# Kernel optimization log

Hardware: AMD Instinct MI355X
Metric: run time of the kernel (lower is better)

Reference implementation:

```python
import jax, jax.numpy as jnp
import numpy as np

B, T, DQ, DV, A, F, K = 64, 1024, 1024, 512, 512, 32, 31


def setup_inputs() -> dict:
    key = jax.random.key(0)
    ks = jax.random.split(key, 8)
    query = jax.random.normal(ks[0], (B, DQ), jnp.float32)
    values = jax.random.normal(ks[1], (B, T, DV), jnp.float32)
    # decoder-step states (as produced by init_states)
    attention_cum = jnp.zeros((B, T), jnp.float32)
    attention_old = jnp.zeros((B, T), jnp.float32)
    alpha = jnp.concatenate([jnp.ones((B, 1), jnp.float32),
                             jnp.zeros((B, T - 1), jnp.float32) + 1e-7], axis=1)
    # learned parameters (Glorot-ish scaling)
    W_query = jax.random.normal(ks[2], (DQ, A), jnp.float32) / np.sqrt(DQ)
    W_inputs = jax.random.normal(ks[3], (DV, A), jnp.float32) / np.sqrt(DV)
    v_w = jax.random.normal(ks[4], (A, 1), jnp.float32) / np.sqrt(A)
    v_b = jnp.zeros((1,), jnp.float32)
    loc_kernel = jax.random.normal(ks[5], (K, 2, F), jnp.float32) / np.sqrt(K * 2)  # WIO
    W_loc = jax.random.normal(ks[6], (F, A), jnp.float32) / np.sqrt(F)
    return {"query": query, "values": values, "attention_cum": attention_cum,
            "attention_old": attention_old, "alpha": alpha,
            "W_query": W_query, "W_inputs": W_inputs, "v_w": v_w, "v_b": v_b,
            "loc_kernel": loc_kernel, "W_loc": W_loc}


def reference(query, values, attention_cum, attention_old, alpha,
              W_query, W_inputs, v_w, v_b, loc_kernel, W_loc):
    # process_values: cached projection of encoder memory  [B,T,A]
    processed_values = jnp.einsum('btd,da->bta', values, W_inputs)
    # location features: conv over stacked (old, cum) attention  [B,T,2]->[B,T,F]
    attn_cat = jnp.stack([attention_old, attention_cum], axis=2)
    conv = jax.lax.conv_general_dilated(attn_cat, loc_kernel, window_strides=(1,),
                                        padding='SAME',
                                        dimension_numbers=('NWC', 'WIO', 'NWC'))
    processed_attn = jnp.einsum('btf,fa->bta', conv, W_loc)
    # query projection  [B,1,A]
    processed_query = (query @ W_query)[:, None, :]
    # additive score  [B,T]
    score = (jnp.tanh(processed_values + processed_query + processed_attn) @ v_w)[..., 0] + v_b
    scores_norm = jax.nn.softmax(score, axis=-1)
    # forward attention recursion
    fwd_shifted = jnp.pad(alpha[:, :-1], ((0, 0), (1, 0)))
    new_alpha = (0.5 * alpha + 0.5 * fwd_shifted + 1e-8) * scores_norm
    new_alpha = new_alpha / jnp.sum(new_alpha, axis=1, keepdims=True)
    attn_weights = new_alpha
    # updated states
    new_cum = attention_cum + scores_norm
    new_old = attn_weights
    # context vector  [B,DV]
    context = jnp.einsum('bt,btd->bd', attn_weights, values)
    return (context, attn_weights, new_cum, new_old, new_alpha)
```

## Files before the change

### kernel.cpp

```cpp
#include <hip/hip_runtime.h>
#include <hip/hip_bf16.h>
#include <cstdint>
#include <cstddef>

#define B 64
#define T 1024
#define DQ 1024
#define DV 512
#define A_DIM 512
#define F_DIM 32
#define KW 31
#define M_TOT (B*T)
#define KEXT2 576
#define NCH 9

typedef __attribute__((ext_vector_type(8))) short short8;
typedef __attribute__((ext_vector_type(4))) float f32x4;

static __device__ __forceinline__ unsigned short f2bf(float f) {
    unsigned int u = __builtin_bit_cast(unsigned int, f);
    u += 0x7fffu + ((u >> 16) & 1u);
    return (unsigned short)(u >> 16);
}
static __device__ __forceinline__ short8 pack8(float4 x0, float4 x1) {
    short8 pk;
    pk[0] = (short)f2bf(x0.x); pk[1] = (short)f2bf(x0.y);
    pk[2] = (short)f2bf(x0.z); pk[3] = (short)f2bf(x0.w);
    pk[4] = (short)f2bf(x1.x); pk[5] = (short)f2bf(x1.y);
    pk[6] = (short)f2bf(x1.z); pk[7] = (short)f2bf(x1.w);
    return pk;
}
static __device__ __forceinline__ float tanh_fast(float x) {
    float e = __expf(2.0f * x);
    return 1.0f - 2.0f * __builtin_amdgcn_rcpf(e + 1.0f);
}

#define LDSDMA16(gptr, lptr)                                                        \
    __builtin_amdgcn_global_load_lds(                                               \
        (const __attribute__((address_space(1))) void*)(const void*)(gptr),         \
        (__attribute__((address_space(3))) void*)(void*)(lptr), 16, 0, 0)

__global__ void prep_kernel(const float* __restrict__ query, const float* __restrict__ Wq,
                            const float* __restrict__ Wi, const float* __restrict__ Wl,
                            const float* __restrict__ old_, const float* __restrict__ cum_,
                            const float* __restrict__ lk,
                            float* __restrict__ pq,
                            float* __restrict__ score, unsigned short* __restrict__ Bt,
                            unsigned short* __restrict__ convb) {
    __shared__ __align__(16) char smem[16640];
    int bid = blockIdx.x, tid = threadIdx.x;
    if (bid < 512) {
        float (*red)[64] = (float(*)[64])smem;
        int pid = bid;
        int gid = pid * 256 + tid;
        if (gid < M_TOT) score[gid] = 0.f;
        int b = pid >> 3, a0 = (pid & 7) * 64;
        int al = tid & 63, ks = tid >> 6;
        const float* qr = query + (size_t)b * DQ + ks * 256;
        const float* wc = Wq + (size_t)(ks * 256) * A_DIM + a0 + al;
        float acc = 0.f;
        #pragma unroll 8
        for (int k = 0; k < 256; ++k) acc += qr[k] * wc[(size_t)k * A_DIM];
        red[ks][al] = acc;
        __syncthreads();
        if (ks == 0)
            pq[b * A_DIM + a0 + al] = red[0][al] + red[1][al] + red[2][al] + red[3][al];
    } else if (bid < 584) {
        float (*tile)[65] = (float(*)[65])smem;
        int tb = bid - 512;
        if (tb < 64) {
            int k0 = (tb >> 3) * 64, a0 = (tb & 7) * 64;
            int al = tid & 63, ko = tid >> 6;
            #pragma unroll
            for (int j = 0; j < 16; ++j) {
                int kl = j * 4 + ko;
                tile[kl][al] = Wi[(size_t)(k0 + kl) * A_DIM + a0 + al];
            }
            __syncthreads();
            int kl2 = tid & 63, ao = tid >> 6;
            #pragma unroll
            for (int j = 0; j < 16; ++j) {
                int al2 = j * 4 + ao;
                Bt[(size_t)(a0 + al2) * KEXT2 + k0 + kl2] = f2bf(tile[kl2][al2]);
            }
        } else {
            int a0 = (tb - 64) * 64;
            int al = tid & 63, ko = tid >> 6;
            #pragma unroll
            for (int j = 0; j < 8; ++j) {
                int kl = j * 4 + ko;
                tile[kl][al] = Wl[(size_t)kl * A_DIM + a0 + al];
            }
            __syncthreads();
            int kl2 = tid & 31, ao = tid >> 5;
            #pragma unroll
            for (int j = 0; j < 8; ++j) {
                int al2 = j * 8 + ao;
                Bt[(size_t)(a0 + al2) * KEXT2 + DV + kl2] = f2bf(tile[kl2][al2]);
            }
            #pragma unroll
            for (int j = 0; j < 8; ++j) {
                int idx = j * 256 + tid;
                int a_l = idx >> 5, kp = idx & 31;
                Bt[(size_t)(a0 + a_l) * KEXT2 + 544 + kp] = 0;
            }
        }
    } else {
        float* sOld = (float*)smem;
        float* sCum = sOld + 94;
        float* sLK  = sCum + 94;
        int cid = bid - 584;
        int b = cid >> 4, t0 = (cid & 15) * 64;
        int tl = tid & 63, fg = tid >> 6;
        for (int j = tid; j < 94; j += 256) {
            int tt = t0 - 15 + j;
            bool ok = (tt >= 0 && tt < T);
            sOld[j] = ok ? old_[b * T + tt] : 0.f;
            sCum[j] = ok ? cum_[b * T + tt] : 0.f;
        }
        for (int j = tid; j < KW * 2 * F_DIM; j += 256) sLK[j] = lk[j];
        __syncthreads();
        float acc[8];
        #pragma unroll
        for (int f = 0; f < 8; ++f) acc[f] = 0.f;
        for (int k = 0; k < KW; ++k) {
            float o = sOld[tl + k], c = sCum[tl + k];
            const float* lo = &sLK[(k * 2 + 0) * F_DIM + fg * 8];
            const float* lc = &sLK[(k * 2 + 1) * F_DIM + fg * 8];
            #pragma unroll
            for (int f = 0; f < 8; ++f) acc[f] += o * lo[f] + c * lc[f];
        }
        short8 pk;
        #pragma unroll
        for (int f = 0; f < 8; ++f) pk[f] = (short)f2bf(acc[f]);
        unsigned short* dst = convb + (size_t)(b * T + t0 + tl) * 64 + fg * 8;
        *(short8*)dst = pk;
        *(short8*)(dst + 32) = (short8)0;
    }
}

__launch_bounds__(256, 3)
__global__ void gemm_score(const float* __restrict__ values,
                           const unsigned short* __restrict__ Bt,
                           const unsigned short* __restrict__ convb,
                           const float* __restrict__ pq,
                           const float* __restrict__ vw,
                           float* __restrict__ score) {
    __shared__ __align__(16) short sA[128 * 64];
    __shared__ __align__(16) short sB[128 * 64];
    __shared__ float sPQ[128];
    __shared__ float sVW[128];
    int tid = threadIdx.x;
    int x = blockIdx.x & 7, l = blockIdx.x >> 3;
    int mt = x * 64 + (l >> 2), nq = l & 3;
    int m0 = mt * 128, n0 = nq * 128;
    int b = m0 >> 10;
    if (tid < 128) { sPQ[tid] = pq[b * A_DIM + n0 + tid]; sVW[tid] = vw[n0 + tid]; }
    int w = tid >> 6, lane = tid & 63, q = lane >> 4, l15 = lane & 15;
    int wm = w & 1, wn = w >> 1;
    const float* aSrc[4];
    int aSlot[4];
    #pragma unroll
    for (int jj = 0; jj < 4; ++jj) {
        int slot = tid * 4 + jj;
        int row = slot >> 3, sl = slot & 7, seg = (sl - row) & 7;
        aSrc[jj] = values + (size_t)(m0 + row) * DV + seg * 8;
        aSlot[jj] = slot;
    }
    f32x4 acc[4][4];
    #pragma unroll
    for (int mi = 0; mi < 4; ++mi)
        #pragma unroll
        for (int ni = 0; ni < 4; ++ni) acc[mi][ni] = (f32x4)0.f;

    for (int c = 0; c < NCH; ++c) {
        __syncthreads();
        #pragma unroll
        for (int j = 0; j < 4; ++j) {
            int slot = j * 256 + tid;
            int row = slot >> 3, seg = ((slot & 7) - row) & 7;
            const unsigned short* gB = Bt + (size_t)(n0 + row) * KEXT2 + c * 64 + seg * 8;
            LDSDMA16(gB, &sB[(j * 256 + w * 64) * 8]);
        }
        if (c < 8) {
            float4 x0[4], x1[4];
            #pragma unroll
            for (int jj = 0; jj < 4; ++jj) {
                const float* s0 = aSrc[jj] + c * 64;
                x0[jj] = *(const float4*)s0;
                x1[jj] = *(const float4*)(s0 + 4);
            }
            #pragma unroll
            for (int jj = 0; jj < 4; ++jj)
                *(short8*)&sA[aSlot[jj] * 8] = pack8(x0[jj], x1[jj]);
        } else {
            #pragma unroll
            for (int j = 0; j < 4; ++j) {
                int slot = j * 256 + tid;
                int row = slot >> 3, seg = ((slot & 7) - row) & 7;
                LDSDMA16(convb + (size_t)(m0 + row) * 64 + seg * 8,
                         &sA[(j * 256 + w * 64) * 8]);
            }
        }
        __syncthreads();
        #pragma unroll
        for (int h = 0; h < 2; ++h) {
            short8 af[4], bfr[4];
            int sgl = h * 4 + q;
            #pragma unroll
            for (int mi = 0; mi < 4; ++mi) {
                int r = wm * 64 + mi * 16 + l15;
                af[mi] = *(const short8*)&sA[r * 64 + (((sgl + r) & 7) << 3)];
            }
            #pragma unroll
            for (int ni = 0; ni < 4; ++ni) {
                int r = wn * 64 + ni * 16 + l15;
                bfr[ni] = *(const short8*)&sB[r * 64 + (((sgl + r) & 7) << 3)];
            }
            #pragma unroll
            for (int mi = 0; mi < 4; ++mi)
                #pragma unroll
                for (int ni = 0; ni < 4; ++ni)
                    acc[mi][ni] = __builtin_amdgcn_mfma_f32_16x16x32_bf16(af[mi], bfr[ni], acc[mi][ni], 0, 0, 0);
        }
    }
    #pragma unroll
    for (int mi = 0; mi < 4; ++mi) {
        #pragma unroll
        for (int r = 0; r < 4; ++r) {
            float s = 0.f;
            #pragma unroll
            for (int ni = 0; ni < 4; ++ni) {
                int col = wn * 64 + ni * 16 + l15;
                float xv = acc[mi][ni][r] + sPQ[col];
                s += tanh_fast(xv) * sVW[col];
            }
            #pragma unroll
            for (int off = 1; off < 16; off <<= 1) s += __shfl_xor(s, off, 64);
            if (l15 == 0)
                atomicAdd(&score[m0 + wm * 64 + mi * 16 + q * 4 + r], s);
        }
    }
}

__global__ void softmax_fwd(const float* __restrict__ score,
                            const float* __restrict__ alpha,
                            const float* __restrict__ cum,
                            float* __restrict__ out) {
    int b = blockIdx.x, t = threadIdx.x;
    __shared__ float sred[16];
    __shared__ float sbc;
    float sc = score[b * T + t];
    int wid = t >> 6, lane = t & 63;
    float m = sc;
    #pragma unroll
    for (int off = 32; off; off >>= 1) m = fmaxf(m, __shfl_xor(m, off, 64));
    if (lane == 0) sred[wid] = m;
    __syncthreads();
    if (t == 0) { float mm = sred[0]; for (int i = 1; i < 16; ++i) mm = fmaxf(mm, sred[i]); sbc = mm; }
    __syncthreads();
    float M = sbc;
    float e = __expf(sc - M);
    float s = e;
    #pragma unroll
    for (int off = 32; off; off >>= 1) s += __shfl_xor(s, off, 64);
    __syncthreads();
    if (lane == 0) sred[wid] = s;
    __syncthreads();
    if (t == 0) { float ss = 0.f; for (int i = 0; i < 16; ++i) ss += sred[i]; sbc = ss; }
    __syncthreads();
    float sn = e / sbc;
    float a_t = alpha[b * T + t];
    float a_p = (t > 0) ? alpha[b * T + t - 1] : 0.f;
    float ua = (0.5f * (a_t + a_p) + 1e-8f) * sn;
    float u = ua;
    #pragma unroll
    for (int off = 32; off; off >>= 1) u += __shfl_xor(u, off, 64);
    __syncthreads();
    if (lane == 0) sred[wid] = u;
    __syncthreads();
    if (t == 0) { float ss = 0.f; for (int i = 0; i < 16; ++i) ss += sred[i]; sbc = ss; }
    __syncthreads();
    float wgt = ua / sbc;
    float* attnw  = out + B * DV;
    float* ncum   = attnw + B * T;
    float* nold   = ncum + B * T;
    float* nalpha = nold + B * T;
    attnw[b * T + t]  = wgt;
    ncum[b * T + t]   = cum[b * T + t] + sn;
    nold[b * T + t]   = wgt;
    nalpha[b * T + t] = wgt;
    if (t < DV) out[b * DV + t] = 0.f;
}

__global__ void context_kernel(const float* __restrict__ values,
                               float* __restrict__ out) {
    __shared__ float red[4][256];
    const float* attnw = out + B * DV;
    int b = blockIdx.x >> 3, tq = (blockIdx.x >> 1) & 3, dh = blockIdx.x & 1;
    int sub = threadIdx.x >> 6, dg = threadIdx.x & 63;
    int t0 = tq * 256 + sub * 64;
    int d0 = dh * 256 + dg * 4;
    float acc[4];
    #pragma unroll
    for (int f = 0; f < 4; ++f) acc[f] = 0.f;
    for (int tt = 0; tt < 64; ++tt) {
        int t = t0 + tt;
        float wgt = attnw[b * T + t];
        float4 xv = *(const float4*)(values + (size_t)(b * T + t) * DV + d0);
        acc[0] += wgt * xv.x; acc[1] += wgt * xv.y;
        acc[2] += wgt * xv.z; acc[3] += wgt * xv.w;
    }
    #pragma unroll
    for (int f = 0; f < 4; ++f) red[sub][dg * 4 + f] = acc[f];
    __syncthreads();
    if (sub == 0) {
        #pragma unroll
        for (int f = 0; f < 4; ++f) {
            int di = dg * 4 + f;
            float s = red[0][di] + red[1][di] + red[2][di] + red[3][di];
            atomicAdd(&out[b * DV + dh * 256 + di], s);
        }
    }
}

extern "C" void kernel_launch(void* const* d_in, const int* in_sizes, int n_in,
                              void* d_out, int out_size, void* d_ws, size_t ws_size,
                              hipStream_t stream) {
    const float* query  = (const float*)d_in[0];
    const float* values = (const float*)d_in[1];
    const float* cum    = (const float*)d_in[2];
    const float* old_   = (const float*)d_in[3];
    const float* alpha  = (const float*)d_in[4];
    const float* Wq     = (const float*)d_in[5];
    const float* Wi     = (const float*)d_in[6];
    const float* vw     = (const float*)d_in[7];
    const float* lk     = (const float*)d_in[9];
    const float* Wl     = (const float*)d_in[10];
    float* out = (float*)d_out;
    char* ws = (char*)d_ws;
    float* ws_pq            = (float*)(ws);
    float* ws_score         = (float*)(ws + 131072);
    unsigned short* ws_Bt   = (unsigned short*)(ws + 393216);
    unsigned short* ws_conv = (unsigned short*)(ws + 1048576);

    prep_kernel<<<1608, 256, 0, stream>>>(query, Wq, Wi, Wl, old_, cum, lk,
                                          ws_pq, ws_score, ws_Bt, ws_conv);
    gemm_score<<<2048, 256, 0, stream>>>(values, ws_Bt, ws_conv, ws_pq, vw, ws_score);
    softmax_fwd<<<64, 1024, 0, stream>>>(ws_score, alpha, cum, out);
    context_kernel<<<512, 256, 0, stream>>>(values, out);
}
```

Baseline: 324.3 us.

## Double-buffer LDS tiles in gemm_score to overlap loads with MFMA

```diff
diff --git a/kernel.cpp b/kernel.cpp
--- a/kernel.cpp
+++ b/kernel.cpp
@@ -139,15 +139,15 @@
     }
 }
 
-__launch_bounds__(256, 3)
+__launch_bounds__(256, 2)
 __global__ void gemm_score(const float* __restrict__ values,
                            const unsigned short* __restrict__ Bt,
                            const unsigned short* __restrict__ convb,
                            const float* __restrict__ pq,
                            const float* __restrict__ vw,
                            float* __restrict__ score) {
-    __shared__ __align__(16) short sA[128 * 64];
-    __shared__ __align__(16) short sB[128 * 64];
+    __shared__ __align__(16) short sA[2][128 * 64];
+    __shared__ __align__(16) short sB[2][128 * 64];
     __shared__ float sPQ[128];
     __shared__ float sVW[128];
     int tid = threadIdx.x;
@@ -159,13 +159,15 @@
     int w = tid >> 6, lane = tid & 63, q = lane >> 4, l15 = lane & 15;
     int wm = w & 1, wn = w >> 1;
     const float* aSrc[4];
+    const unsigned short* bSrc[4];
     int aSlot[4];
     #pragma unroll
-    for (int jj = 0; jj < 4; ++jj) {
-        int slot = tid * 4 + jj;
-        int row = slot >> 3, sl = slot & 7, seg = (sl - row) & 7;
-        aSrc[jj] = values + (size_t)(m0 + row) * DV + seg * 8;
-        aSlot[jj] = slot;
+    for (int j = 0; j < 4; ++j) {
+        int slot = j * 256 + tid;
+        int row = slot >> 3, seg = ((slot & 7) - row) & 7;
+        aSrc[j] = values + (size_t)(m0 + row) * DV + seg * 8;
+        bSrc[j] = Bt + (size_t)(n0 + row) * KEXT2 + seg * 8;
+        aSlot[j] = slot;
     }
     f32x4 acc[4][4];
     #pragma unroll
@@ -173,36 +175,47 @@
         #pragma unroll
         for (int ni = 0; ni < 4; ++ni) acc[mi][ni] = (f32x4)0.f;
 
+    {
+        float4 px0[4], px1[4];
+        #pragma unroll
+        for (int j = 0; j < 4; ++j) {
+            px0[j] = *(const float4*)(aSrc[j]);
+            px1[j] = *(const float4*)(aSrc[j] + 4);
+        }
+        #pragma unroll
+        for (int j = 0; j < 4; ++j)
+            LDSDMA16(bSrc[j], &sB[0][(j * 256 + w * 64) * 8]);
+        #pragma unroll
+        for (int j = 0; j < 4; ++j)
+            *(short8*)&sA[0][aSlot[j] * 8] = pack8(px0[j], px1[j]);
+    }
+    __syncthreads();
+
+    int cur = 0;
     for (int c = 0; c < NCH; ++c) {
-        __syncthreads();
-        #pragma unroll
-        for (int j = 0; j < 4; ++j) {
-            int slot = j * 256 + tid;
-            int row = slot >> 3, seg = ((slot & 7) - row) & 7;
-            const unsigned short* gB = Bt + (size_t)(n0 + row) * KEXT2 + c * 64 + seg * 8;
-            LDSDMA16(gB, &sB[(j * 256 + w * 64) * 8]);
-        }
-        if (c < 8) {
-            float4 x0[4], x1[4];
-            #pragma unroll
-            for (int jj = 0; jj < 4; ++jj) {
-                const float* s0 = aSrc[jj] + c * 64;
-                x0[jj] = *(const float4*)s0;
-                x1[jj] = *(const float4*)(s0 + 4);
-            }
-            #pragma unroll
-            for (int jj = 0; jj < 4; ++jj)
-                *(short8*)&sA[aSlot[jj] * 8] = pack8(x0[jj], x1[jj]);
-        } else {
-            #pragma unroll
-            for (int j = 0; j < 4; ++j) {
-                int slot = j * 256 + tid;
-                int row = slot >> 3, seg = ((slot & 7) - row) & 7;
-                LDSDMA16(convb + (size_t)(m0 + row) * 64 + seg * 8,
-                         &sA[(j * 256 + w * 64) * 8]);
-            }
-        }
-        __syncthreads();
+        int nxt = cur ^ 1;
+        float4 nx0[4], nx1[4];
+        if (c + 1 < NCH) {
+            if (c + 1 < 8) {
+                #pragma unroll
+                for (int j = 0; j < 4; ++j) {
+                    const float* s0 = aSrc[j] + (c + 1) * 64;
+                    nx0[j] = *(const float4*)s0;
+                    nx1[j] = *(const float4*)(s0 + 4);
+                }
+            } else {
+                #pragma unroll
+                for (int j = 0; j < 4; ++j) {
+                    int slot = j * 256 + tid;
+                    int row = slot >> 3, seg = ((slot & 7) - row) & 7;
+                    LDSDMA16(convb + (size_t)(m0 + row) * 64 + seg * 8,
+                             &sA[nxt][(j * 256 + w * 64) * 8]);
+                }
+            }
+            #pragma unroll
+            for (int j = 0; j < 4; ++j)
+                LDSDMA16(bSrc[j] + (c + 1) * 64, &sB[nxt][(j * 256 + w * 64) * 8]);
+        }
         #pragma unroll
         for (int h = 0; h < 2; ++h) {
             short8 af[4], bfr[4];
@@ -210,12 +223,12 @@
             #pragma unroll
             for (int mi = 0; mi < 4; ++mi) {
                 int r = wm * 64 + mi * 16 + l15;
-                af[mi] = *(const short8*)&sA[r * 64 + (((sgl + r) & 7) << 3)];
+                af[mi] = *(const short8*)&sA[cur][r * 64 + (((sgl + r) & 7) << 3)];
             }
             #pragma unroll
             for (int ni = 0; ni < 4; ++ni) {
                 int r = wn * 64 + ni * 16 + l15;
-                bfr[ni] = *(const short8*)&sB[r * 64 + (((sgl + r) & 7) << 3)];
+                bfr[ni] = *(const short8*)&sB[cur][r * 64 + (((sgl + r) & 7) << 3)];
             }
             #pragma unroll
             for (int mi = 0; mi < 4; ++mi)
@@ -223,6 +236,13 @@
                 for (int ni = 0; ni < 4; ++ni)
                     acc[mi][ni] = __builtin_amdgcn_mfma_f32_16x16x32_bf16(af[mi], bfr[ni], acc[mi][ni], 0, 0, 0);
         }
+        if (c + 1 < 8) {
+            #pragma unroll
+            for (int j = 0; j < 4; ++j)
+                *(short8*)&sA[nxt][aSlot[j] * 8] = pack8(nx0[j], nx1[j]);
+        }
+        __syncthreads();
+        cur ^= 1;
     }
     #pragma unroll
     for (int mi = 0; mi < 4; ++mi) {
```

Measured after the change: 319.1 us. No clear change (-1.6%).

## Stage fp32 values into LDS via async DMA and convert at fragment load

Applied to the files above, without the earlier changes.

```diff
diff --git a/kernel.cpp b/kernel.cpp
--- a/kernel.cpp
+++ b/kernel.cpp
@@ -22,17 +22,22 @@
     u += 0x7fffu + ((u >> 16) & 1u);
     return (unsigned short)(u >> 16);
 }
-static __device__ __forceinline__ short8 pack8(float4 x0, float4 x1) {
-    short8 pk;
-    pk[0] = (short)f2bf(x0.x); pk[1] = (short)f2bf(x0.y);
-    pk[2] = (short)f2bf(x0.z); pk[3] = (short)f2bf(x0.w);
-    pk[4] = (short)f2bf(x1.x); pk[5] = (short)f2bf(x1.y);
-    pk[6] = (short)f2bf(x1.z); pk[7] = (short)f2bf(x1.w);
-    return pk;
-}
 static __device__ __forceinline__ float tanh_fast(float x) {
     float e = __expf(2.0f * x);
     return 1.0f - 2.0f * __builtin_amdgcn_rcpf(e + 1.0f);
+}
+static __device__ __forceinline__ unsigned cvtpk(float lo, float hi) {
+    return (unsigned)f2bf(lo) | ((unsigned)f2bf(hi) << 16);
+}
+static __device__ __forceinline__ short8 cvt8(f32x4 a, f32x4 b) {
+    unsigned u0 = cvtpk(a[0], a[1]), u1 = cvtpk(a[2], a[3]);
+    unsigned u2 = cvtpk(b[0], b[1]), u3 = cvtpk(b[2], b[3]);
+    short8 r;
+    r[0] = (short)(u0 & 0xffff); r[1] = (short)(u0 >> 16);
+    r[2] = (short)(u1 & 0xffff); r[3] = (short)(u1 >> 16);
+    r[4] = (short)(u2 & 0xffff); r[5] = (short)(u2 >> 16);
+    r[6] = (short)(u3 & 0xffff); r[7] = (short)(u3 >> 16);
+    return r;
 }
 
 #define LDSDMA16(gptr, lptr)                                                        \
@@ -146,7 +151,7 @@
                            const float* __restrict__ pq,
                            const float* __restrict__ vw,
                            float* __restrict__ score) {
-    __shared__ __align__(16) short sA[128 * 64];
+    __shared__ __align__(16) float sAf[128 * 64];
     __shared__ __align__(16) short sB[128 * 64];
     __shared__ float sPQ[128];
     __shared__ float sVW[128];
@@ -158,15 +163,12 @@
     if (tid < 128) { sPQ[tid] = pq[b * A_DIM + n0 + tid]; sVW[tid] = vw[n0 + tid]; }
     int w = tid >> 6, lane = tid & 63, q = lane >> 4, l15 = lane & 15;
     int wm = w & 1, wn = w >> 1;
-    const float* aSrc[4];
-    int aSlot[4];
-    #pragma unroll
-    for (int jj = 0; jj < 4; ++jj) {
-        int slot = tid * 4 + jj;
-        int row = slot >> 3, sl = slot & 7, seg = (sl - row) & 7;
-        aSrc[jj] = values + (size_t)(m0 + row) * DV + seg * 8;
-        aSlot[jj] = slot;
-    }
+    int trow = tid >> 4, pA = tid & 15;
+    const float* aBase = values + (size_t)(m0 + trow) * DV + (pA ^ trow) * 4;
+    int brow = tid >> 3, bseg = ((tid & 7) - brow) & 7;
+    const unsigned short* bBase = Bt + (size_t)(n0 + brow) * KEXT2 + bseg * 8;
+    const unsigned short* cBase = convb + (size_t)(m0 + brow) * 64 + bseg * 8;
+
     f32x4 acc[4][4];
     #pragma unroll
     for (int mi = 0; mi < 4; ++mi)
@@ -175,47 +177,46 @@
 
     for (int c = 0; c < NCH; ++c) {
         __syncthreads();
-        #pragma unroll
-        for (int j = 0; j < 4; ++j) {
-            int slot = j * 256 + tid;
-            int row = slot >> 3, seg = ((slot & 7) - row) & 7;
-            const unsigned short* gB = Bt + (size_t)(n0 + row) * KEXT2 + c * 64 + seg * 8;
-            LDSDMA16(gB, &sB[(j * 256 + w * 64) * 8]);
-        }
         if (c < 8) {
-            float4 x0[4], x1[4];
-            #pragma unroll
-            for (int jj = 0; jj < 4; ++jj) {
-                const float* s0 = aSrc[jj] + c * 64;
-                x0[jj] = *(const float4*)s0;
-                x1[jj] = *(const float4*)(s0 + 4);
-            }
-            #pragma unroll
-            for (int jj = 0; jj < 4; ++jj)
-                *(short8*)&sA[aSlot[jj] * 8] = pack8(x0[jj], x1[jj]);
+            #pragma unroll
+            for (int j = 0; j < 8; ++j)
+                LDSDMA16(aBase + (size_t)j * 16 * DV + c * 64,
+                         &sAf[(j * 256 + w * 64) * 4]);
         } else {
             #pragma unroll
-            for (int j = 0; j < 4; ++j) {
-                int slot = j * 256 + tid;
-                int row = slot >> 3, seg = ((slot & 7) - row) & 7;
-                LDSDMA16(convb + (size_t)(m0 + row) * 64 + seg * 8,
-                         &sA[(j * 256 + w * 64) * 8]);
-            }
-        }
+            for (int j = 0; j < 4; ++j)
+                LDSDMA16(cBase + j * 32 * 64,
+                         (short*)sAf + (j * 256 + w * 64) * 8);
+        }
+        #pragma unroll
+        for (int j = 0; j < 4; ++j)
+            LDSDMA16(bBase + (size_t)j * 32 * KEXT2 + c * 64,
+                     &sB[(j * 256 + w * 64) * 8]);
         __syncthreads();
         #pragma unroll
         for (int h = 0; h < 2; ++h) {
             short8 af[4], bfr[4];
-            int sgl = h * 4 + q;
-            #pragma unroll
-            for (int mi = 0; mi < 4; ++mi) {
-                int r = wm * 64 + mi * 16 + l15;
-                af[mi] = *(const short8*)&sA[r * 64 + (((sgl + r) & 7) << 3)];
-            }
             #pragma unroll
             for (int ni = 0; ni < 4; ++ni) {
                 int r = wn * 64 + ni * 16 + l15;
-                bfr[ni] = *(const short8*)&sB[r * 64 + (((sgl + r) & 7) << 3)];
+                bfr[ni] = *(const short8*)&sB[r * 64 + ((((h * 4 + q) + r) & 7) << 3)];
+            }
+            if (c < 8) {
+                #pragma unroll
+                for (int mi = 0; mi < 4; ++mi) {
+                    int r = wm * 64 + mi * 16 + l15;
+                    int ps = (h * 8 + q * 2) ^ l15;
+                    f32x4 lo = *(const f32x4*)&sAf[r * 64 + ps * 4];
+                    f32x4 hi = *(const f32x4*)&sAf[r * 64 + (ps ^ 1) * 4];
+                    af[mi] = cvt8(lo, hi);
+                }
+            } else {
+                const short* sAh = (const short*)sAf;
+                #pragma unroll
+                for (int mi = 0; mi < 4; ++mi) {
+                    int r = wm * 64 + mi * 16 + l15;
+                    af[mi] = *(const short8*)&sAh[r * 64 + ((((h * 4 + q) + r) & 7) << 3)];
+                }
             }
             #pragma unroll
             for (int mi = 0; mi < 4; ++mi)
@@ -297,14 +298,14 @@
                                float* __restrict__ out) {
     __shared__ float red[4][256];
     const float* attnw = out + B * DV;
-    int b = blockIdx.x >> 3, tq = (blockIdx.x >> 1) & 3, dh = blockIdx.x & 1;
+    int b = blockIdx.x >> 5, tq = (blockIdx.x >> 1) & 15, dh = blockIdx.x & 1;
     int sub = threadIdx.x >> 6, dg = threadIdx.x & 63;
-    int t0 = tq * 256 + sub * 64;
+    int t0 = tq * 64 + sub * 16;
     int d0 = dh * 256 + dg * 4;
     float acc[4];
     #pragma unroll
     for (int f = 0; f < 4; ++f) acc[f] = 0.f;
-    for (int tt = 0; tt < 64; ++tt) {
+    for (int tt = 0; tt < 16; ++tt) {
         int t = t0 + tt;
         float wgt = attnw[b * T + t];
         float4 xv = *(const float4*)(values + (size_t)(b * T + t) * DV + d0);
@@ -348,5 +349,5 @@
                                           ws_pq, ws_score, ws_Bt, ws_conv);
     gemm_score<<<2048, 256, 0, stream>>>(values, ws_Bt, ws_conv, ws_pq, vw, ws_score);
     softmax_fwd<<<64, 1024, 0, stream>>>(ws_score, alpha, cum, out);
-    context_kernel<<<512, 256, 0, stream>>>(values, out);
-}
+    context_kernel<<<2048, 256, 0, stream>>>(values, out);
+}
```

Result: faster. 298.9 us (-7.8%).
